# Kernel tuning notes

Hardware: AMD Instinct MI355X
Metric: run time of the kernel (lower is better)

## Reference

```python
import jax, jax.numpy as jnp
import numpy as np

H = 16
D_MODEL = 1024
D_K = D_MODEL // H


def setup_inputs() -> dict:
    key = jax.random.key(0)
    ks = jax.random.split(key, 12)
    B, S = 4, 2048
    scale = 1.0 / np.sqrt(D_MODEL)
    inp = {
        "query": jax.random.normal(ks[0], (B, S, D_MODEL), dtype=jnp.float32),
        "key": jax.random.normal(ks[1], (B, S, D_MODEL), dtype=jnp.float32),
        "value": jax.random.normal(ks[2], (B, S, D_MODEL), dtype=jnp.float32),
        "Wq": jax.random.normal(ks[3], (D_MODEL, D_MODEL), dtype=jnp.float32) * scale,
        "bq": jnp.zeros((D_MODEL,), dtype=jnp.float32),
        "Wk": jax.random.normal(ks[4], (D_MODEL, D_MODEL), dtype=jnp.float32) * scale,
        "bk": jnp.zeros((D_MODEL,), dtype=jnp.float32),
        "Wv": jax.random.normal(ks[5], (D_MODEL, D_MODEL), dtype=jnp.float32) * scale,
        "bv": jnp.zeros((D_MODEL,), dtype=jnp.float32),
        "Wo": jax.random.normal(ks[6], (D_MODEL, D_MODEL), dtype=jnp.float32) * scale,
        "bo": jnp.zeros((D_MODEL,), dtype=jnp.float32),
    }
    return inp


def reference(query, key, value, Wq, bq, Wk, bk, Wv, bv, Wo, bo):
    B, S, _ = query.shape
    # Linear projections (torch Linear: x @ W^T + b), then split heads -> [B,H,S,d_k]
    def proj(x, W, b):
        y = x @ W.T + b
        return y.reshape(B, S, H, D_K).transpose(0, 2, 1, 3)

    q = proj(query, Wq, bq)
    k = proj(key, Wk, bk)
    v = proj(value, Wv, bv)

    # Explicit QK^T / sqrt(d_k), softmax, AV (no mask; dropout = identity in eval)
    scores = jnp.einsum("bhqd,bhkd->bhqk", q, k) / jnp.sqrt(jnp.float32(D_K))
    attn = jax.nn.softmax(scores, axis=-1)
    x = jnp.einsum("bhqk,bhkd->bhqd", attn, v)

    # Merge heads and final output projection
    x = x.transpose(0, 2, 1, 3).reshape(B, S, H * D_K)
    return x @ Wo.T + bo
```

## Files before the change

kernel.cpp:

```cpp
#include <hip/hip_runtime.h>
#include <hip/hip_bf16.h>
#include <stdint.h>

#define BATCH 4
#define SEQ   2048
#define DM    1024
#define NH    16
#define DK    64
#define MROWS (BATCH * SEQ)

#define C1 0.1803368801111204f

typedef __attribute__((ext_vector_type(8))) short short8;
typedef __attribute__((ext_vector_type(4))) float f32x4;
typedef __attribute__((ext_vector_type(4))) float floatv4;
typedef __attribute__((ext_vector_type(4))) unsigned short us4;
typedef __attribute__((ext_vector_type(4))) unsigned int uint4v;

static __device__ __forceinline__ unsigned short f2bf(float f) {
    union { float f; uint32_t u; } c; c.f = f;
    uint32_t u = c.u;
    return (unsigned short)((u + 0x7fffu + ((u >> 16) & 1u)) >> 16);
}

static __device__ __forceinline__ unsigned int cvt_pk_bf16(float a, float b) {
    __hip_bfloat162 h = __float22bfloat162_rn(float2{a, b});
    unsigned int u; __builtin_memcpy(&u, &h, 4); return u;
}

static __device__ __forceinline__ float ex2(float x) { return __builtin_amdgcn_exp2f(x); }

#define AS1C(p) ((const __attribute__((address_space(1))) unsigned int*)(uintptr_t)(const void*)(p))
#define AS3(p)  ((__attribute__((address_space(3))) unsigned int*)(uintptr_t)(void*)(p))

__global__ __launch_bounds__(256) void cvt3_k(const float* __restrict__ a, const float* __restrict__ b,
                                              const float* __restrict__ c,
                                              unsigned short* __restrict__ oa, unsigned short* __restrict__ ob,
                                              unsigned short* __restrict__ oc) {
    const int z = blockIdx.y;
    const float* s = (z == 0) ? a : (z == 1) ? b : c;
    unsigned short* o = (z == 0) ? oa : (z == 1) ? ob : oc;
    int i = blockIdx.x * 256 + threadIdx.x;
    floatv4 v = ((const floatv4*)s)[i];
    us4 w; w.x = f2bf(v.x); w.y = f2bf(v.y); w.z = f2bf(v.z); w.w = f2bf(v.w);
    ((us4*)o)[i] = w;
}

__global__ __launch_bounds__(256) void cvt4_k(const float* __restrict__ a, const float* __restrict__ b,
                                              const float* __restrict__ c, const float* __restrict__ d,
                                              unsigned short* __restrict__ oa, unsigned short* __restrict__ ob,
                                              unsigned short* __restrict__ oc, unsigned short* __restrict__ od) {
    const int z = blockIdx.y;
    const float* s = (z == 0) ? a : (z == 1) ? b : (z == 2) ? c : d;
    unsigned short* o = (z == 0) ? oa : (z == 1) ? ob : (z == 2) ? oc : od;
    int i = blockIdx.x * 256 + threadIdx.x;
    floatv4 v = ((const floatv4*)s)[i];
    us4 w; w.x = f2bf(v.x); w.y = f2bf(v.y); w.z = f2bf(v.z); w.w = f2bf(v.w);
    ((us4*)o)[i] = w;
}

static __device__ __forceinline__ void gemm_body(const unsigned short* __restrict__ A,
                                                 const unsigned short* __restrict__ Bw,
                                                 const float* __restrict__ bias,
                                                 void* __restrict__ out, int m0, int n0,
                                                 float scale, int mode) {
    constexpr int K = DM;
    constexpr int NK = K / 32;

    const int tid = threadIdx.x;
    const int wave = tid >> 6, lane = tid & 63, quad = lane >> 4, l16 = lane & 15;
    const int wm = wave >> 1, wn = wave & 1;

    __shared__ alignas(16) unsigned short As[2][256 * 32];
    __shared__ alignas(16) unsigned short Bs[2][128 * 32];

    f32x4 acc[4][4];
    #pragma unroll
    for (int i = 0; i < 4; i++)
        #pragma unroll
        for (int j = 0; j < 4; j++) acc[i][j] = (f32x4){0.f, 0.f, 0.f, 0.f};

    const int scol8 = (((lane & 3) ^ ((lane >> 3) & 3))) * 8;
    const unsigned short* Ag0 = A  + (size_t)(m0 + wave * 32 + (lane >> 2)) * K + scol8;
    const unsigned short* Ag1 = Ag0 + (size_t)16 * K;
    const unsigned short* Bg0 = Bw + (size_t)(n0 + wave * 16 + (lane >> 2)) * K + scol8;

    const int rsw = (quad ^ ((l16 >> 1) & 3)) * 8;

    short8 af[4], bfr[4];

#define GX_STG(b, kt)                                                                     \
    {   __builtin_amdgcn_global_load_lds(AS1C(Ag0 + (size_t)(kt) * 32),                   \
                                         AS3(&As[b][(wave * 32) * 32]), 16, 0, 0);        \
        __builtin_amdgcn_global_load_lds(AS1C(Ag1 + (size_t)(kt) * 32),                   \
                                         AS3(&As[b][(wave * 32 + 16) * 32]), 16, 0, 0);   \
        __builtin_amdgcn_global_load_lds(AS1C(Bg0 + (size_t)(kt) * 32),                   \
                                         AS3(&Bs[b][(wave * 16) * 32]), 16, 0, 0); }

#define GX_LD(b)                                                                          \
    {   _Pragma("unroll")                                                                 \
        for (int i_ = 0; i_ < 4; i_++) af[i_]  = *(const short8*)&As[b][(wm * 64 + i_ * 16 + l16) * 32 + rsw]; \
        _Pragma("unroll")                                                                 \
        for (int j_ = 0; j_ < 4; j_++) bfr[j_] = *(const short8*)&Bs[b][(wn * 64 + j_ * 16 + l16) * 32 + rsw]; }

#define GX_MMA                                                                            \
    {   __builtin_amdgcn_s_setprio(1);                                                    \
        _Pragma("unroll")                                                                 \
        for (int i_ = 0; i_ < 4; i_++)                                                    \
            _Pragma("unroll")                                                             \
            for (int j_ = 0; j_ < 4; j_++)                                                \
                acc[i_][j_] = __builtin_amdgcn_mfma_f32_16x16x32_bf16(af[i_], bfr[j_], acc[i_][j_], 0, 0, 0); \
        __builtin_amdgcn_s_setprio(0); }

#define GX_VM0  { asm volatile("s_waitcnt vmcnt(0)" ::: "memory"); }
#define GX_BAR  __builtin_amdgcn_s_barrier()
#define GX_SB0  __builtin_amdgcn_sched_barrier(0)
#define GX_LG0  { asm volatile("s_waitcnt lgkmcnt(0)" ::: "memory"); __builtin_amdgcn_sched_barrier(0); }

    GX_STG(0, 0);
    #pragma unroll 1
    for (int k = 0; k < NK; k += 2) {
        GX_VM0; GX_BAR; GX_SB0;
        GX_STG(1, k + 1);
        GX_LD(0); GX_LG0; GX_MMA;
        GX_VM0; GX_BAR; GX_SB0;
        if (k + 2 < NK) GX_STG(0, k + 2);
        GX_LD(1); GX_LG0; GX_MMA;
    }

#undef GX_STG
#undef GX_LD
#undef GX_MMA
#undef GX_VM0
#undef GX_BAR
#undef GX_SB0
#undef GX_LG0

    #pragma unroll
    for (int nf = 0; nf < 4; nf++) {
        const int n = n0 + wn * 64 + nf * 16 + l16;
        const float bv = bias[n];
        if (mode == 2) {
            const int bb = m0 >> 11;
            const int hh = n >> 6, dd = n & (DK - 1);
            unsigned short* obase = (unsigned short*)out
                                  + (((size_t)bb * NH + hh) * DK + dd) * SEQ
                                  + (m0 & (SEQ - 1)) + wm * 64 + quad * 8;
            #pragma unroll
            for (int mf = 0; mf < 4; mf++) {
                us4 w;
                #pragma unroll
                for (int r = 0; r < 4; r++) w[r] = f2bf(acc[mf][nf][r] + bv);
                *(us4*)(obase + (mf >> 1) * 32 + (mf & 1) * 4) = w;
            }
        } else {
            const int hh = n >> 6, dd = n & (DK - 1);
            #pragma unroll
            for (int mf = 0; mf < 4; mf++) {
                #pragma unroll
                for (int r = 0; r < 4; r++) {
                    const int mrow = m0 + wm * 64 + mf * 16 + quad * 4 + r;
                    float val = (acc[mf][nf][r] + bv) * scale;
                    if (mode == 0) {
                        int bb = mrow >> 11, ss = mrow & (SEQ - 1);
                        ((unsigned short*)out)[((((size_t)bb * NH + hh) * SEQ + ss) << 6) + dd] = f2bf(val);
                    } else {
                        ((float*)out)[(size_t)mrow * DM + n] = val;
                    }
                }
            }
        }
    }
}

__global__ __launch_bounds__(512, 4) void gemm_qkv_k(const unsigned short* qa, const unsigned short* ka,
                                                     const unsigned short* va, const unsigned short* wq,
                                                     const unsigned short* wk, const unsigned short* wv,
                                                     const float* bq, const float* bk, const float* bv,
                                                     unsigned short* qh, unsigned short* kh,
                                                     unsigned short* vtc) {
    const int z = blockIdx.z;
    const unsigned short* A = (z == 0) ? qa : (z == 1) ? ka : va;
    const unsigned short* W = (z == 0) ? wq : (z == 1) ? wk : wv;
    const float* bi = (z == 0) ? bq : (z == 1) ? bk : bv;
    void* o = (z == 0) ? (void*)qh : (z == 1) ? (void*)kh : (void*)vtc;
    const float sc = (z == 0) ? C1 : 1.0f;
    const int mode = (z == 2) ? 2 : 0;
    gemm_body(A, W, bi, o, blockIdx.x * 256, blockIdx.y * 128, sc, mode);
}

__global__ __launch_bounds__(512, 4) void gemm_o_k(const unsigned short* xb, const unsigned short* wo,
                                                   const float* bo, float* out) {
    gemm_body(xb, wo, bo, out, blockIdx.x * 256, blockIdx.y * 128, 1.0f, 1);
}

__global__ __launch_bounds__(256, 2) void flash_attn_k(const unsigned short* __restrict__ Qh,
                                                       const unsigned short* __restrict__ Kh,
                                                       const unsigned short* __restrict__ Vtc,
                                                       unsigned short* __restrict__ Xb) {
    const int tid = threadIdx.x;
    const int wave = tid >> 6, lane = tid & 63, quad = lane >> 4, l16 = lane & 15;
    const int h = blockIdx.y, b = blockIdx.z;
    const unsigned short* Qp = Qh  + (size_t)(b * NH + h) * SEQ * DK;
    const unsigned short* Kp = Kh  + (size_t)(b * NH + h) * SEQ * DK;
    const unsigned short* Vp = Vtc + (size_t)(b * NH + h) * DK * SEQ;
    const int q0 = blockIdx.x * 256 + wave * 64;

    __shared__ alignas(16) unsigned short kt[2][128][72];
    __shared__ alignas(16) unsigned short vt[2][64][136];

    short8 aq[4][2];
    #pragma unroll
    for (int m = 0; m < 4; m++)
        #pragma unroll
        for (int kk = 0; kk < 2; kk++)
            aq[m][kk] = *(const short8*)(Qp + (size_t)(q0 + m * 16 + l16) * DK + kk * 32 + quad * 8);

    short8 ones;
    #pragma unroll
    for (int j = 0; j < 8; j++) ones[j] = (short)0x3F80;

    f32x4 O[4][4];
    f32x4 lacc[4];
    #pragma unroll
    for (int m = 0; m < 4; m++) {
        #pragma unroll
        for (int db = 0; db < 4; db++) O[m][db] = (f32x4){0.f, 0.f, 0.f, 0.f};
        lacc[m] = (f32x4){0.f, 0.f, 0.f, 0.f};
    }

    const unsigned short* kgp = Kp + (size_t)(tid >> 3) * DK + (tid & 7) * 8;
    const unsigned short* vgp = Vp + (size_t)(tid >> 4) * SEQ + (tid & 15) * 8;
    unsigned short* kws0 = &kt[0][tid >> 3][(tid & 7) * 8];
    unsigned short* vws0 = &vt[0][tid >> 4][(tid & 15) * 8];

    short8 krg[4], vrg[4];
    #pragma unroll
    for (int it = 0; it < 4; it++) {
        krg[it] = *(const short8*)(kgp + (size_t)it * 32 * DK);
        vrg[it] = *(const short8*)(vgp + (size_t)it * 16 * SEQ);
    }
    kgp += (size_t)128 * DK;
    vgp += 128;
    #pragma unroll
    for (int it = 0; it < 4; it++) {
        *(short8*)(kws0 + it * 32 * 72) = krg[it];
        *(short8*)(vws0 + it * 16 * 136) = vrg[it];
    }
    #pragma unroll
    for (int it = 0; it < 4; it++) {
        krg[it] = *(const short8*)(kgp + (size_t)it * 32 * DK);
        vrg[it] = *(const short8*)(vgp + (size_t)it * 16 * SEQ);
    }
    kgp += (size_t)128 * DK;
    vgp += 128;
    asm volatile("s_waitcnt lgkmcnt(0)" ::: "memory");
    __builtin_amdgcn_s_barrier();
    __builtin_amdgcn_sched_barrier(0);

#define FLASH_TILE(cur)                                                                   \
    {   _Pragma("unroll")                                                                 \
        for (int it = 0; it < 4; it++) {                                                  \
            *(short8*)(kws0 + ((cur) ^ 1) * 128 * 72 + it * 32 * 72) = krg[it];           \
            *(short8*)(vws0 + ((cur) ^ 1) * 64 * 136 + it * 16 * 136) = vrg[it];          \
        }                                                                                 \
        _Pragma("unroll")                                                                 \
        for (int it = 0; it < 4; it++) {                                                  \
            krg[it] = *(const short8*)(kgp + (size_t)it * 32 * DK);                       \
            vrg[it] = *(const short8*)(vgp + (size_t)it * 16 * SEQ);                      \
        }                                                                                 \
        kgp += (size_t)128 * DK;                                                          \
        vgp += 128;                                                                       \
        _Pragma("unroll")                                                                 \
        for (int t = 0; t < 4; t++) {                                                     \
            f32x4 s[4][2];                                                                \
            _Pragma("unroll")                                                             \
            for (int m = 0; m < 4; m++) {                                                 \
                s[m][0] = (f32x4){0.f, 0.f, 0.f, 0.f};                                    \
                s[m][1] = (f32x4){0.f, 0.f, 0.f, 0.f};                                    \
            }                                                                             \
            _Pragma("unroll")                                                             \
            for (int kk = 0; kk < 2; kk++) {                                              \
                short8 bk0 = *(const short8*)&kt[cur][(t * 2    ) * 16 + l16][kk * 32 + quad * 8]; \
                short8 bk1 = *(const short8*)&kt[cur][(t * 2 + 1) * 16 + l16][kk * 32 + quad * 8]; \
                _Pragma("unroll")                                                         \
                for (int m = 0; m < 4; m++) {                                             \
                    s[m][0] = __builtin_amdgcn_mfma_f32_16x16x32_bf16(bk0, aq[m][kk], s[m][0], 0, 0, 0); \
                    s[m][1] = __builtin_amdgcn_mfma_f32_16x16x32_bf16(bk1, aq[m][kk], s[m][1], 0, 0, 0); \
                }                                                                         \
            }                                                                             \
            short8 pa[4];                                                                 \
            _Pragma("unroll")                                                             \
            for (int m = 0; m < 4; m++) {                                                 \
                uint4v pk;                                                                \
                pk.x = cvt_pk_bf16(ex2(s[m][0][0]), ex2(s[m][0][1]));                     \
                pk.y = cvt_pk_bf16(ex2(s[m][0][2]), ex2(s[m][0][3]));                     \
                pk.z = cvt_pk_bf16(ex2(s[m][1][0]), ex2(s[m][1][1]));                     \
                pk.w = cvt_pk_bf16(ex2(s[m][1][2]), ex2(s[m][1][3]));                     \
                __builtin_memcpy(&pa[m], &pk, 16);                                        \
            }                                                                             \
            _Pragma("unroll")                                                             \
            for (int db = 0; db < 4; db++) {                                              \
                short8 vf = *(const short8*)&vt[cur][db * 16 + l16][t * 32 + quad * 8];   \
                _Pragma("unroll")                                                         \
                for (int m = 0; m < 4; m++)                                               \
                    O[m][db] = __builtin_amdgcn_mfma_f32_16x16x32_bf16(pa[m], vf, O[m][db], 0, 0, 0); \
            }                                                                             \
            _Pragma("unroll")                                                             \
            for (int m = 0; m < 4; m++)                                                   \
                lacc[m] = __builtin_amdgcn_mfma_f32_16x16x32_bf16(pa[m], ones, lacc[m], 0, 0, 0); \
        }                                                                                 \
        asm volatile("s_waitcnt lgkmcnt(0)" ::: "memory");                                \
        __builtin_amdgcn_s_barrier();                                                     \
        __builtin_amdgcn_sched_barrier(0);                                                \
    }

    #pragma unroll 1
    for (int ti = 0; ti < SEQ / 128; ti += 2) {
        FLASH_TILE(0);
        FLASH_TILE(1);
    }
#undef FLASH_TILE

    #pragma unroll
    for (int m = 0; m < 4; m++) {
        #pragma unroll
        for (int r = 0; r < 4; r++) {
            const float inv = 1.f / lacc[m][r];
            const int srow = q0 + m * 16 + quad * 4 + r;
            unsigned short* op = Xb + ((size_t)b * SEQ + srow) * DM + h * DK;
            #pragma unroll
            for (int db = 0; db < 4; db++)
                op[db * 16 + l16] = f2bf(O[m][db][r] * inv);
        }
    }
}

extern "C" void kernel_launch(void* const* d_in, const int* in_sizes, int n_in,
                              void* d_out, int out_size, void* d_ws, size_t ws_size,
                              hipStream_t stream) {
    const float* q_in = (const float*)d_in[0];
    const float* k_in = (const float*)d_in[1];
    const float* v_in = (const float*)d_in[2];
    const float* Wq   = (const float*)d_in[3];
    const float* bq   = (const float*)d_in[4];
    const float* Wk   = (const float*)d_in[5];
    const float* bk   = (const float*)d_in[6];
    const float* Wv   = (const float*)d_in[7];
    const float* bv   = (const float*)d_in[8];
    const float* Wo   = (const float*)d_in[9];
    const float* bo   = (const float*)d_in[10];

    const size_t MB = 1024ull * 1024ull;
    char* ws = (char*)d_ws;
    unsigned short* qa  = (unsigned short*)(ws +   0 * MB);
    unsigned short* ka  = (unsigned short*)(ws +  16 * MB);
    unsigned short* va  = (unsigned short*)(ws +  32 * MB);
    unsigned short* wqb = (unsigned short*)(ws +  48 * MB);
    unsigned short* wkb = (unsigned short*)(ws +  50 * MB);
    unsigned short* wvb = (unsigned short*)(ws +  52 * MB);
    unsigned short* wob = (unsigned short*)(ws +  54 * MB);
    unsigned short* qh  = (unsigned short*)(ws +  56 * MB);
    unsigned short* kh  = (unsigned short*)(ws +  72 * MB);
    unsigned short* vtc = (unsigned short*)(ws +  88 * MB);
    unsigned short* xb  = (unsigned short*)(ws + 104 * MB);

    cvt3_k<<<dim3(8192, 3), 256, 0, stream>>>(q_in, k_in, v_in, qa, ka, va);
    cvt4_k<<<dim3(1024, 4), 256, 0, stream>>>(Wq, Wk, Wv, Wo, wqb, wkb, wvb, wob);

    gemm_qkv_k<<<dim3(MROWS / 256, DM / 128, 3), 512, 0, stream>>>(qa, ka, va, wqb, wkb, wvb,
                                                                   bq, bk, bv, qh, kh, vtc);

    flash_attn_k<<<dim3(SEQ / 256, NH, BATCH), 256, 0, stream>>>(qh, kh, vtc, xb);

    gemm_o_k<<<dim3(MROWS / 256, DM / 128), 512, 0, stream>>>(xb, wob, bo, (float*)d_out);
}
```

Measured before the change: 334.5 us.

## Software-pipeline QK^T and exp/PV across sub-tiles with MFMA priority hints

Splits each 128-key tile into S (QK^T) and exp+PV stages, then double-buffers the score registers (sA/sB) so the QK^T MFMAs of sub-tile t+1 are issued before the exp/PV work of sub-tile t. The first score block is computed before the global-to-LDS staging stores. MFMA groups are wrapped in s_setprio(1)/0 so the matrix units stay fed while other waves do exp and conversion. This adds 32 accumulator registers per lane, which may raise register pressure and reduce occupancy.

New measurement: 340.2 us. No clear change (+1.7%).

```diff
diff --git a/kernel.cpp b/kernel.cpp
--- a/kernel.cpp
+++ b/kernel.cpp
@@ -222,6 +222,7 @@
 
     f32x4 O[4][4];
     f32x4 lacc[4];
+    f32x4 sA[4][2], sB[4][2];
     #pragma unroll
     for (int m = 0; m < 4; m++) {
         #pragma unroll
@@ -258,8 +259,54 @@
     __builtin_amdgcn_s_barrier();
     __builtin_amdgcn_sched_barrier(0);
 
+#define FL_S(sv, cur, t)                                                                  \
+    {   _Pragma("unroll")                                                                 \
+        for (int m = 0; m < 4; m++) { sv[m][0] = (f32x4){0.f,0.f,0.f,0.f};                \
+                                      sv[m][1] = (f32x4){0.f,0.f,0.f,0.f}; }              \
+        _Pragma("unroll")                                                                 \
+        for (int kk = 0; kk < 2; kk++) {                                                  \
+            short8 bk0 = *(const short8*)&kt[cur][((t) * 2    ) * 16 + l16][kk * 32 + quad * 8]; \
+            short8 bk1 = *(const short8*)&kt[cur][((t) * 2 + 1) * 16 + l16][kk * 32 + quad * 8]; \
+            __builtin_amdgcn_s_setprio(1);                                                \
+            _Pragma("unroll")                                                             \
+            for (int m = 0; m < 4; m++) {                                                 \
+                sv[m][0] = __builtin_amdgcn_mfma_f32_16x16x32_bf16(bk0, aq[m][kk], sv[m][0], 0, 0, 0); \
+                sv[m][1] = __builtin_amdgcn_mfma_f32_16x16x32_bf16(bk1, aq[m][kk], sv[m][1], 0, 0, 0); \
+            }                                                                             \
+            __builtin_amdgcn_s_setprio(0);                                                \
+        }                                                                                 \
+    }
+
+#define FL_EPV(sv, cur, t)                                                                \
+    {   short8 pa[4];                                                                     \
+        _Pragma("unroll")                                                                 \
+        for (int m = 0; m < 4; m++) {                                                     \
+            uint4v pk;                                                                    \
+            pk.x = cvt_pk_bf16(ex2(sv[m][0][0]), ex2(sv[m][0][1]));                       \
+            pk.y = cvt_pk_bf16(ex2(sv[m][0][2]), ex2(sv[m][0][3]));                       \
+            pk.z = cvt_pk_bf16(ex2(sv[m][1][0]), ex2(sv[m][1][1]));                       \
+            pk.w = cvt_pk_bf16(ex2(sv[m][1][2]), ex2(sv[m][1][3]));                       \
+            __builtin_memcpy(&pa[m], &pk, 16);                                            \
+        }                                                                                 \
+        _Pragma("unroll")                                                                 \
+        for (int db = 0; db < 4; db++) {                                                  \
+            short8 vf = *(const short8*)&vt[cur][db * 16 + l16][(t) * 32 + quad * 8];     \
+            __builtin_amdgcn_s_setprio(1);                                                \
+            _Pragma("unroll")                                                             \
+            for (int m = 0; m < 4; m++)                                                   \
+                O[m][db] = __builtin_amdgcn_mfma_f32_16x16x32_bf16(pa[m], vf, O[m][db], 0, 0, 0); \
+            __builtin_amdgcn_s_setprio(0);                                                \
+        }                                                                                 \
+        __builtin_amdgcn_s_setprio(1);                                                    \
+        _Pragma("unroll")                                                                 \
+        for (int m = 0; m < 4; m++)                                                       \
+            lacc[m] = __builtin_amdgcn_mfma_f32_16x16x32_bf16(pa[m], ones, lacc[m], 0, 0, 0); \
+        __builtin_amdgcn_s_setprio(0);                                                    \
+    }
+
 #define FLASH_TILE(cur)                                                                   \
-    {   _Pragma("unroll")                                                                 \
+    {   FL_S(sA, cur, 0);                                                                 \
+        _Pragma("unroll")                                                                 \
         for (int it = 0; it < 4; it++) {                                                  \
             *(short8*)(kws0 + ((cur) ^ 1) * 128 * 72 + it * 32 * 72) = krg[it];           \
             *(short8*)(vws0 + ((cur) ^ 1) * 64 * 136 + it * 16 * 136) = vrg[it];          \
@@ -271,45 +318,10 @@
         }                                                                                 \
         kgp += (size_t)128 * DK;                                                          \
         vgp += 128;                                                                       \
-        _Pragma("unroll")                                                                 \
-        for (int t = 0; t < 4; t++) {                                                     \
-            f32x4 s[4][2];                                                                \
-            _Pragma("unroll")                                                             \
-            for (int m = 0; m < 4; m++) {                                                 \
-                s[m][0] = (f32x4){0.f, 0.f, 0.f, 0.f};                                    \
-                s[m][1] = (f32x4){0.f, 0.f, 0.f, 0.f};                                    \
-            }                                                                             \
-            _Pragma("unroll")                                                             \
-            for (int kk = 0; kk < 2; kk++) {                                              \
-                short8 bk0 = *(const short8*)&kt[cur][(t * 2    ) * 16 + l16][kk * 32 + quad * 8]; \
-                short8 bk1 = *(const short8*)&kt[cur][(t * 2 + 1) * 16 + l16][kk * 32 + quad * 8]; \
-                _Pragma("unroll")                                                         \
-                for (int m = 0; m < 4; m++) {                                             \
-                    s[m][0] = __builtin_amdgcn_mfma_f32_16x16x32_bf16(bk0, aq[m][kk], s[m][0], 0, 0, 0); \
-                    s[m][1] = __builtin_amdgcn_mfma_f32_16x16x32_bf16(bk1, aq[m][kk], s[m][1], 0, 0, 0); \
-                }                                                                         \
-            }                                                                             \
-            short8 pa[4];                                                                 \
-            _Pragma("unroll")                                                             \
-            for (int m = 0; m < 4; m++) {                                                 \
-                uint4v pk;                                                                \
-                pk.x = cvt_pk_bf16(ex2(s[m][0][0]), ex2(s[m][0][1]));                     \
-                pk.y = cvt_pk_bf16(ex2(s[m][0][2]), ex2(s[m][0][3]));                     \
-                pk.z = cvt_pk_bf16(ex2(s[m][1][0]), ex2(s[m][1][1]));                     \
-                pk.w = cvt_pk_bf16(ex2(s[m][1][2]), ex2(s[m][1][3]));                     \
-                __builtin_memcpy(&pa[m], &pk, 16);                                        \
-            }                                                                             \
-            _Pragma("unroll")                                                             \
-            for (int db = 0; db < 4; db++) {                                              \
-                short8 vf = *(const short8*)&vt[cur][db * 16 + l16][t * 32 + quad * 8];   \
-                _Pragma("unroll")                                                         \
-                for (int m = 0; m < 4; m++)                                               \
-                    O[m][db] = __builtin_amdgcn_mfma_f32_16x16x32_bf16(pa[m], vf, O[m][db], 0, 0, 0); \
-            }                                                                             \
-            _Pragma("unroll")                                                             \
-            for (int m = 0; m < 4; m++)                                                   \
-                lacc[m] = __builtin_amdgcn_mfma_f32_16x16x32_bf16(pa[m], ones, lacc[m], 0, 0, 0); \
-        }                                                                                 \
+        FL_S(sB, cur, 1); FL_EPV(sA, cur, 0);                                             \
+        FL_S(sA, cur, 2); FL_EPV(sB, cur, 1);                                             \
+        FL_S(sB, cur, 3); FL_EPV(sA, cur, 2);                                             \
+        FL_EPV(sB, cur, 3);                                                               \
         asm volatile("s_waitcnt lgkmcnt(0)" ::: "memory");                                \
         __builtin_amdgcn_s_barrier();                                                     \
         __builtin_amdgcn_sched_barrier(0);                                                \
@@ -321,6 +333,8 @@
         FLASH_TILE(1);
     }
 #undef FLASH_TILE
+#undef FL_S
+#undef FL_EPV
 
     #pragma unroll
     for (int m = 0; m < 4; m++) {
```
